# Optimization experiments

Hardware: AMD Instinct MI355X
Metric: run time of the kernel (lower is better)

## Reference

```python
import jax, jax.numpy as jnp
import numpy as np

B, S, D, H = 2, 2048, 1024, 16
DH = D // H  # 64


def setup_inputs() -> dict:
    key = jax.random.key(0)
    ks = jax.random.split(key, 8)
    query = jax.random.normal(ks[0], (B, S, D), jnp.float32)
    k_in = jax.random.normal(ks[1], (B, S, D), jnp.float32)
    v_in = jax.random.normal(ks[2], (B, S, D), jnp.float32)
    mask = jnp.zeros((B, 1, 1, S), jnp.float32)  # padding mask (0 = keep)
    # distance-based attention penalty mask: |i-j| normalized
    idx = jnp.arange(S, dtype=jnp.float32)
    att_pen_mask = jnp.abs(idx[:, None] - idx[None, :])[None, None] / S
    scale = 1.0 / np.sqrt(D)
    Wq = jax.random.normal(ks[3], (D, D), jnp.float32) * scale
    Wk = jax.random.normal(ks[4], (D, D), jnp.float32) * scale
    Wv = jax.random.normal(ks[5], (D, D), jnp.float32) * scale
    Wo = jax.random.normal(ks[6], (D, D), jnp.float32) * scale
    bo = jnp.zeros((D,), jnp.float32)
    return {"query": query, "key": k_in, "value": v_in, "mask": mask,
            "att_pen_mask": att_pen_mask, "attention_dropout": 0,
            "Wq": Wq, "Wk": Wk, "Wv": Wv, "Wo": Wo, "bo": bo}


def _split_heads(x):
    # [B,S,D] -> [B,H,S,DH]
    return x.reshape(B, S, H, DH).transpose(0, 2, 1, 3)


def reference(query, key, value, mask, att_pen_mask, attention_dropout, Wq, Wk, Wv, Wo, bo):
    q = _split_heads(query @ Wq)
    k = _split_heads(key @ Wk)
    v = _split_heads(value @ Wv)
    # scaled dot-product attention with penalty + padding mask
    scores = jnp.einsum('bhqd,bhkd->bhqk', q, k) / jnp.sqrt(jnp.float32(DH))
    scores = scores - jnp.log1p(att_pen_mask)          # distance penalty
    scores = scores + mask * (-1e9)                    # padding mask
    attn = jax.nn.softmax(scores, axis=-1)
    # attention_dropout==0 -> no dropout (matches 0 < rate < 1 gate)
    ctx = jnp.einsum('bhqk,bhkd->bhqd', attn, v)       # [B,H,S,DH]
    ctx = ctx.transpose(0, 2, 1, 3).reshape(B, S, D)
    out = ctx @ Wo + bo
    return out, attn
```

## Files before the change

### kernel.cpp

```cpp
#include <hip/hip_runtime.h>
#include <math.h>

#define BB 2
#define SS 2048
#define DD 1024
#define HH 16
#define DHH 64

typedef _Float16 f16;
typedef f16 f16x8 __attribute__((ext_vector_type(8)));
typedef f16 f16x4 __attribute__((ext_vector_type(4)));
typedef float f32x4 __attribute__((ext_vector_type(4)));
typedef float fvec4 __attribute__((ext_vector_type(4)));

#define LOG2E 1.4426950408889634f

static __device__ __forceinline__ f32x4 mfma16(f16x8 a, f16x8 b, f32x4 c) {
    return __builtin_amdgcn_mfma_f32_16x16x32_f16(a, b, c, 0, 0, 0);
}

#define SWZ(r, c) ((c) ^ (((r) & 7) << 3))

static __device__ __forceinline__ void gload_lds16(const void* g, void* l) {
    __builtin_amdgcn_global_load_lds(
        (const __attribute__((address_space(1))) void*)g,
        (__attribute__((address_space(3))) void*)l, 16, 0, 0);
}

static __device__ __forceinline__ void barrier_raw() {
    __builtin_amdgcn_sched_barrier(0);
    __builtin_amdgcn_s_barrier();
    __builtin_amdgcn_sched_barrier(0);
}
static __device__ __forceinline__ void barrier_lds() {
    asm volatile("s_waitcnt lgkmcnt(0)" ::: "memory");
    __builtin_amdgcn_s_barrier();
    __builtin_amdgcn_sched_barrier(0);
}

__global__ __launch_bounds__(256) void wtrans_kernel(
    const float* __restrict__ w0, const float* __restrict__ w1,
    const float* __restrict__ w2, const float* __restrict__ w3,
    f16* __restrict__ o0, f16* __restrict__ o1,
    f16* __restrict__ o2, f16* __restrict__ o3)
{
    const float* src; f16* dst;
    switch (blockIdx.z) {
        case 0:  src = w0; dst = o0; break;
        case 1:  src = w1; dst = o1; break;
        case 2:  src = w2; dst = o2; break;
        default: src = w3; dst = o3; break;
    }
    __shared__ float t[64][65];
    const int tid = threadIdx.x;
    const int n0 = blockIdx.x * 64, k0 = blockIdx.y * 64;
    const int r = tid >> 4, c4 = (tid & 15) * 4;
    #pragma unroll
    for (int p = 0; p < 4; ++p) {
        int row = r + p * 16;
        fvec4 v = *(const fvec4*)&src[(size_t)(k0 + row) * DD + n0 + c4];
        #pragma unroll
        for (int j = 0; j < 4; ++j) t[row][c4 + j] = v[j];
    }
    __syncthreads();
    #pragma unroll
    for (int p = 0; p < 4; ++p) {
        int row = r + p * 16;
        f16x4 v;
        #pragma unroll
        for (int j = 0; j < 4; ++j) v[j] = (f16)t[c4 + j][row];
        *(f16x4*)&dst[(size_t)(n0 + row) * DD + k0 + c4] = v;
    }
}

__global__ __launch_bounds__(256) void gemm_qkv(
    const float* __restrict__ Aq, const float* __restrict__ Ak, const float* __restrict__ Av,
    const f16* __restrict__ Wqt, const f16* __restrict__ Wkt, const f16* __restrict__ Wvt,
    f16* __restrict__ oq, f16* __restrict__ ok, f16* __restrict__ ovt)
{
    const int K = DD;
    const int l = (blockIdx.x & 7) * 96 + (blockIdx.x >> 3);
    const int z  = (l % 96) / 32;
    const int mt = (l / 96) * 4 + (l % 32) / 8;
    const int nt = l % 8;

    const float* A; const f16* Bt; f16* C;
    switch (z) {
        case 0:  A = Aq; Bt = Wqt; C = oq; break;
        case 1:  A = Ak; Bt = Wkt; C = ok; break;
        default: A = Av; Bt = Wvt; C = ovt; break;
    }
    const int m0 = mt * 128, n0 = nt * 128;
    const int tid = threadIdx.x, lane = tid & 63;
    const int wm = (tid >> 7) & 1, wn = (tid >> 6) & 1;
    const int ln = lane & 15, lg = lane >> 4;

    __shared__ f16 As[128 * 64];
    __shared__ f16 Bs[128 * 64];

    f32x4 acc[4][4] = {};

    const int sr = tid >> 3;
    const int sc = (tid & 7) * 8;
    const int l8 = sr & 7;
    const int bsrc = ((tid & 7) ^ l8) * 8;
    const int ldsbase = (sr & ~7) * 64;

    for (int k0 = 0; k0 < K; k0 += 64) {
        #pragma unroll
        for (int p = 0; p < 4; ++p)
            gload_lds16(Bt + (size_t)(n0 + sr + p * 32) * K + k0 + bsrc,
                        &Bs[ldsbase + p * 32 * 64]);
        #pragma unroll
        for (int p = 0; p < 4; ++p) {
            int row = sr + p * 32;
            const float* s = A + (size_t)(m0 + row) * K + k0 + sc;
            fvec4 x0 = *(const fvec4*)s;
            fvec4 x1 = *(const fvec4*)(s + 4);
            f16x8 v;
            #pragma unroll
            for (int j = 0; j < 4; ++j) { v[j] = (f16)x0[j]; v[j + 4] = (f16)x1[j]; }
            *(f16x8*)&As[row * 64 + SWZ(row, sc)] = v;
        }
        __syncthreads();
        #pragma unroll
        for (int ks = 0; ks < 2; ++ks) {
            f16x8 af[4], bf[4];
            #pragma unroll
            for (int i = 0; i < 4; ++i) {
                int ra = wm * 64 + i * 16 + ln, rb = wn * 64 + i * 16 + ln;
                int cc = ks * 32 + lg * 8;
                af[i] = *(const f16x8*)&As[ra * 64 + SWZ(ra, cc)];
                bf[i] = *(const f16x8*)&Bs[rb * 64 + SWZ(rb, cc)];
            }
            __builtin_amdgcn_s_setprio(1);
            #pragma unroll
            for (int i = 0; i < 4; ++i)
                #pragma unroll
                for (int j = 0; j < 4; ++j)
                    acc[i][j] = mfma16(af[i], bf[j], acc[i][j]);
            __builtin_amdgcn_s_setprio(0);
        }
        __syncthreads();
    }

    const int vmode = (z == 2);
    #pragma unroll
    for (int i = 0; i < 4; ++i) {
        #pragma unroll
        for (int j = 0; j < 4; ++j) {
            if (vmode) {
                int m = m0 + wm * 64 + i * 16 + lg * 4;
                int n = n0 + wn * 64 + j * 16 + ln;
                int b = m >> 11, s = m & (SS - 1);
                int h = n >> 6, dh = n & 63;
                f16x4 v4;
                #pragma unroll
                for (int v = 0; v < 4; ++v) v4[v] = (f16)acc[i][j][v];
                *(f16x4*)&C[((size_t)((b * HH + h) * DHH + dh)) * SS + s] = v4;
            } else {
                #pragma unroll
                for (int v = 0; v < 4; ++v) {
                    int m = m0 + wm * 64 + i * 16 + lg * 4 + v;
                    int n = n0 + wn * 64 + j * 16 + ln;
                    int b = m >> 11, s = m & (SS - 1);
                    int h = n >> 6, dh = n & 63;
                    C[((size_t)((b * HH + h) * SS + s)) * DHH + dh] = (f16)acc[i][j][v];
                }
            }
        }
    }
}

__global__ __launch_bounds__(256) void gemm_out(
    const f16* __restrict__ A, const f16* __restrict__ Bt,
    const float* __restrict__ bias, float* __restrict__ C)
{
    const int K = DD;
    const int l = (blockIdx.x & 7) * 32 + (blockIdx.x >> 3);
    const int mt = (l / 32) * 4 + (l % 32) / 8;
    const int nt = l % 8;
    const int m0 = mt * 128, n0 = nt * 128;
    const int tid = threadIdx.x, lane = tid & 63;
    const int wm = (tid >> 7) & 1, wn = (tid >> 6) & 1;
    const int ln = lane & 15, lg = lane >> 4;

    __shared__ f16 As[128 * 64];
    __shared__ f16 Bs[128 * 64];

    f32x4 acc[4][4] = {};

    const int sr = tid >> 3;
    const int l8 = sr & 7;
    const int bsrc = ((tid & 7) ^ l8) * 8;
    const int ldsbase = (sr & ~7) * 64;

    for (int k0 = 0; k0 < K; k0 += 64) {
        #pragma unroll
        for (int p = 0; p < 4; ++p) {
            gload_lds16(A + (size_t)(m0 + sr + p * 32) * K + k0 + bsrc,
                        &As[ldsbase + p * 32 * 64]);
            gload_lds16(Bt + (size_t)(n0 + sr + p * 32) * K + k0 + bsrc,
                        &Bs[ldsbase + p * 32 * 64]);
        }
        __syncthreads();
        #pragma unroll
        for (int ks = 0; ks < 2; ++ks) {
            f16x8 af[4], bf[4];
            #pragma unroll
            for (int i = 0; i < 4; ++i) {
                int ra = wm * 64 + i * 16 + ln, rb = wn * 64 + i * 16 + ln;
                int cc = ks * 32 + lg * 8;
                af[i] = *(const f16x8*)&As[ra * 64 + SWZ(ra, cc)];
                bf[i] = *(const f16x8*)&Bs[rb * 64 + SWZ(rb, cc)];
            }
            __builtin_amdgcn_s_setprio(1);
            #pragma unroll
            for (int i = 0; i < 4; ++i)
                #pragma unroll
                for (int j = 0; j < 4; ++j)
                    acc[i][j] = mfma16(af[i], bf[j], acc[i][j]);
            __builtin_amdgcn_s_setprio(0);
        }
        __syncthreads();
    }

    #pragma unroll
    for (int i = 0; i < 4; ++i)
        #pragma unroll
        for (int j = 0; j < 4; ++j)
            #pragma unroll
            for (int v = 0; v < 4; ++v) {
                int m = m0 + wm * 64 + i * 16 + lg * 4 + v;
                int n = n0 + wn * 64 + j * 16 + ln;
                C[(size_t)m * DD + n] = acc[i][j][v] + bias[n];
            }
}

__global__ __launch_bounds__(256, 4) void attn_kernel(
    const f16* __restrict__ qg, const f16* __restrict__ kg, const f16* __restrict__ vtg,
    const float* __restrict__ maskg, const float* __restrict__ peng,
    float* __restrict__ attn_out, f16* __restrict__ ctx_out)
{
    const int bid = blockIdx.x;
    const int wg = (bid & 7) * 128 + (bid >> 3);
    const int bh = wg >> 5;
    const int b = bh >> 4, h = bh & 15;
    const int q0 = (wg & 31) * 64;

    const int tid = threadIdx.x, lane = tid & 63, wv = tid >> 6;
    const int ln = lane & 15, lg = lane >> 4;

    __shared__ f16 Kt[64 * 64];
    __shared__ f16 Vt[64 * 64];
    __shared__ f16 Ps[64 * 64];
    __shared__ f16 mrowh[SS];

    for (int i = tid; i < SS; i += 256)
        mrowh[i] = (f16)fmaxf(maskg[b * SS + i] * (-1e9f * LOG2E), -60000.f);

    const f16* qbase = qg + ((size_t)bh * SS + q0 + wv * 16 + ln) * DHH;
    f16x8 aq0 = *(const f16x8*)(qbase + lg * 8);
    f16x8 aq1 = *(const f16x8*)(qbase + 32 + lg * 8);

    const f16* kbase = kg + (size_t)bh * SS * DHH;
    const f16* vbase = vtg + (size_t)bh * DHH * SS;

    const int krow = tid >> 3, kcol = (tid & 7) * 8;
    f16x8 kst0, kst1, vst0, vst1;

    #define LOADK(kt) { kst0 = *(const f16x8*)(kbase + ((size_t)(kt) * 64 + krow) * DHH + kcol); \
                        kst1 = *(const f16x8*)(kbase + ((size_t)(kt) * 64 + krow + 32) * DHH + kcol); }
    #define WRITEK()  { *(f16x8*)&Kt[krow * 64 + SWZ(krow, kcol)] = kst0; \
                        *(f16x8*)&Kt[(krow + 32) * 64 + SWZ(krow + 32, kcol)] = kst1; }
    #define LOADV(kt) { vst0 = *(const f16x8*)(vbase + (size_t)krow * SS + (kt) * 64 + kcol); \
                        vst1 = *(const f16x8*)(vbase + (size_t)(krow + 32) * SS + (kt) * 64 + kcol); }
    #define WRITEV()  { *(f16x8*)&Vt[krow * 64 + SWZ(krow, kcol)] = vst0; \
                        *(f16x8*)&Vt[(krow + 32) * 64 + SWZ(krow + 32, kcol)] = vst1; }

    const int q = q0 + wv * 16 + ln;
    const float SC = 0.125f * LOG2E;

    LOADK(0);
    WRITEK();
    __syncthreads();

    float lrun = 0.f;

    for (int kt = 0; kt < 32; ++kt) {
        if (kt < 31) LOADK(kt + 1);

        float sum = 0.f;
        #pragma unroll
        for (int sub = 0; sub < 4; ++sub) {
            int kr = sub * 16 + ln;
            f16x8 k0 = *(const f16x8*)&Kt[kr * 64 + SWZ(kr, lg * 8)];
            f16x8 k1 = *(const f16x8*)&Kt[kr * 64 + SWZ(kr, 32 + lg * 8)];
            f32x4 sa = {0.f, 0.f, 0.f, 0.f};
            __builtin_amdgcn_s_setprio(1);
            sa = mfma16(k0, aq0, sa);
            sa = mfma16(k1, aq1, sa);
            __builtin_amdgcn_s_setprio(0);
            const int kjb = kt * 64 + sub * 16 + lg * 4;
            f16x4 mr = *(const f16x4*)&mrowh[kjb];
            #pragma unroll
            for (int v = 0; v < 4; ++v) {
                int d = q - (kjb + v); d = d < 0 ? -d : d;
                sum += __builtin_amdgcn_exp2f(
                    sa[v] * SC + (float)mr[v] - __builtin_amdgcn_logf((float)(SS + d)));
            }
        }
        sum += __shfl_xor(sum, 16);
        sum += __shfl_xor(sum, 32);
        lrun += sum;

        barrier_raw();
        if (kt < 31) WRITEK();
        barrier_lds();
    }

    const float cfix = __builtin_amdgcn_logf(lrun);

    f32x4 cacc[4] = {};

    LOADK(0); LOADV(0);
    WRITEK(); WRITEV();
    __syncthreads();

    for (int kt = 0; kt < 32; ++kt) {
        if (kt < 31) { LOADK(kt + 1); LOADV(kt + 1); }

        #pragma unroll
        for (int sub = 0; sub < 4; ++sub) {
            int kr = sub * 16 + ln;
            f16x8 k0 = *(const f16x8*)&Kt[kr * 64 + SWZ(kr, lg * 8)];
            f16x8 k1 = *(const f16x8*)&Kt[kr * 64 + SWZ(kr, 32 + lg * 8)];
            f32x4 sa = {0.f, 0.f, 0.f, 0.f};
            __builtin_amdgcn_s_setprio(1);
            sa = mfma16(k0, aq0, sa);
            sa = mfma16(k1, aq1, sa);
            __builtin_amdgcn_s_setprio(0);
            const int kjb = kt * 64 + sub * 16 + lg * 4;
            f16x4 mr = *(const f16x4*)&mrowh[kjb];
            f32x4 p;
            #pragma unroll
            for (int v = 0; v < 4; ++v) {
                int d = q - (kjb + v); d = d < 0 ? -d : d;
                p[v] = __builtin_amdgcn_exp2f(
                    sa[v] * SC + (float)mr[v]
                    - __builtin_amdgcn_logf((float)(SS + d)) - cfix);
            }
            __builtin_nontemporal_store(
                p, (fvec4*)(attn_out + ((size_t)bh * SS + q) * SS + kjb));
            f16x4 pc;
            #pragma unroll
            for (int v = 0; v < 4; ++v) pc[v] = (f16)p[v];
            const int prow = wv * 16 + ln;
            *(f16x4*)&Ps[prow * 64 + SWZ(prow, sub * 16 + lg * 4)] = pc;
        }
        #pragma unroll
        for (int ks = 0; ks < 2; ++ks) {
            const int prow = wv * 16 + ln;
            f16x8 ap = *(const f16x8*)&Ps[prow * 64 + SWZ(prow, ks * 32 + lg * 8)];
            f16x8 bv0 = *(const f16x8*)&Vt[(0 * 16 + ln) * 64 + SWZ(0 * 16 + ln, ks * 32 + lg * 8)];
            f16x8 bv1 = *(const f16x8*)&Vt[(1 * 16 + ln) * 64 + SWZ(1 * 16 + ln, ks * 32 + lg * 8)];
            f16x8 bv2 = *(const f16x8*)&Vt[(2 * 16 + ln) * 64 + SWZ(2 * 16 + ln, ks * 32 + lg * 8)];
            f16x8 bv3 = *(const f16x8*)&Vt[(3 * 16 + ln) * 64 + SWZ(3 * 16 + ln, ks * 32 + lg * 8)];
            __builtin_amdgcn_s_setprio(1);
            cacc[0] = mfma16(ap, bv0, cacc[0]);
            cacc[1] = mfma16(ap, bv1, cacc[1]);
            cacc[2] = mfma16(ap, bv2, cacc[2]);
            cacc[3] = mfma16(ap, bv3, cacc[3]);
            __builtin_amdgcn_s_setprio(0);
        }

        barrier_raw();
        if (kt < 31) { WRITEK(); WRITEV(); }
        barrier_lds();
    }

    #pragma unroll
    for (int nsub = 0; nsub < 4; ++nsub) {
        #pragma unroll
        for (int v = 0; v < 4; ++v) {
            int s = q0 + wv * 16 + lg * 4 + v;
            ctx_out[(size_t)(b * SS + s) * DD + h * DHH + nsub * 16 + ln] = (f16)cacc[nsub][v];
        }
    }
    #undef LOADK
    #undef WRITEK
    #undef LOADV
    #undef WRITEV
}

extern "C" void kernel_launch(void* const* d_in, const int* in_sizes, int n_in,
                              void* d_out, int out_size, void* d_ws, size_t ws_size,
                              hipStream_t stream)
{
    const float* query = (const float*)d_in[0];
    const float* key   = (const float*)d_in[1];
    const float* value = (const float*)d_in[2];
    const float* mask  = (const float*)d_in[3];
    const float* pen   = (const float*)d_in[4];
    const float* Wq = (const float*)d_in[6];
    const float* Wk = (const float*)d_in[7];
    const float* Wv = (const float*)d_in[8];
    const float* Wo = (const float*)d_in[9];
    const float* bo = (const float*)d_in[10];

    char* ws = (char*)d_ws;
    f16* Wqt   = (f16*)(ws);
    f16* Wkt   = (f16*)(ws + (2ull << 20));
    f16* Wvt   = (f16*)(ws + (4ull << 20));
    f16* Wot   = (f16*)(ws + (6ull << 20));
    f16* qbuf  = (f16*)(ws + (8ull << 20));
    f16* kbuf  = (f16*)(ws + (16ull << 20));
    f16* vtbuf = (f16*)(ws + (24ull << 20));
    f16* ctx   = (f16*)(ws + (32ull << 20));

    float* out_main = (float*)d_out;
    float* attn_out = (float*)d_out + (size_t)BB * SS * DD;

    wtrans_kernel<<<dim3(16, 16, 4), 256, 0, stream>>>(Wq, Wk, Wv, Wo, Wqt, Wkt, Wvt, Wot);
    gemm_qkv<<<dim3(768), 256, 0, stream>>>(query, key, value, Wqt, Wkt, Wvt, qbuf, kbuf, vtbuf);
    attn_kernel<<<dim3(1024), 256, 0, stream>>>(qbuf, kbuf, vtbuf, mask, pen, attn_out, ctx);
    gemm_out<<<dim3(256), 256, 0, stream>>>(ctx, Wot, bo, out_main);
}
```

Before: 282.2 us.

## Split attention waves 2x2 over queries and keys, use reciprocal penalty factor

```diff
diff --git a/kernel.cpp b/kernel.cpp
--- a/kernel.cpp
+++ b/kernel.cpp
@@ -248,20 +248,26 @@
     const int b = bh >> 4, h = bh & 15;
     const int q0 = (wg & 31) * 64;
 
-    const int tid = threadIdx.x, lane = tid & 63, wv = tid >> 6;
+    const int tid = threadIdx.x, lane = tid & 63;
+    const int wq = tid >> 7, wk = (tid >> 6) & 1;
     const int ln = lane & 15, lg = lane >> 4;
 
-    __shared__ f16 Kt[64 * 64];
-    __shared__ f16 Vt[64 * 64];
-    __shared__ f16 Ps[64 * 64];
+    __shared__ f16 arena[12288];
     __shared__ f16 mrowh[SS];
+    f16* const Kt = arena;
+    f16* const Vt = arena + 4096;
+    f16* const Ps = arena + 8192;
 
     for (int i = tid; i < SS; i += 256)
         mrowh[i] = (f16)fmaxf(maskg[b * SS + i] * (-1e9f * LOG2E), -60000.f);
 
-    const f16* qbase = qg + ((size_t)bh * SS + q0 + wv * 16 + ln) * DHH;
-    f16x8 aq0 = *(const f16x8*)(qbase + lg * 8);
-    f16x8 aq1 = *(const f16x8*)(qbase + 32 + lg * 8);
+    f16x8 aq0[2], aq1[2];
+    #pragma unroll
+    for (int g = 0; g < 2; ++g) {
+        const f16* qb = qg + ((size_t)bh * SS + q0 + wq * 32 + g * 16 + ln) * DHH;
+        aq0[g] = *(const f16x8*)(qb + lg * 8);
+        aq1[g] = *(const f16x8*)(qb + 32 + lg * 8);
+    }
 
     const f16* kbase = kg + (size_t)bh * SS * DHH;
     const f16* vbase = vtg + (size_t)bh * DHH * SS;
@@ -278,50 +284,67 @@
     #define WRITEV()  { *(f16x8*)&Vt[krow * 64 + SWZ(krow, kcol)] = vst0; \
                         *(f16x8*)&Vt[(krow + 32) * 64 + SWZ(krow + 32, kcol)] = vst1; }
 
-    const int q = q0 + wv * 16 + ln;
     const float SC = 0.125f * LOG2E;
 
     LOADK(0);
     WRITEK();
     __syncthreads();
 
-    float lrun = 0.f;
+    float lsum[2] = {0.f, 0.f};
 
     for (int kt = 0; kt < 32; ++kt) {
         if (kt < 31) LOADK(kt + 1);
 
-        float sum = 0.f;
-        #pragma unroll
-        for (int sub = 0; sub < 4; ++sub) {
-            int kr = sub * 16 + ln;
+        #pragma unroll
+        for (int ksub = 0; ksub < 2; ++ksub) {
+            const int sub = wk * 2 + ksub;
+            const int kr = sub * 16 + ln;
             f16x8 k0 = *(const f16x8*)&Kt[kr * 64 + SWZ(kr, lg * 8)];
             f16x8 k1 = *(const f16x8*)&Kt[kr * 64 + SWZ(kr, 32 + lg * 8)];
-            f32x4 sa = {0.f, 0.f, 0.f, 0.f};
-            __builtin_amdgcn_s_setprio(1);
-            sa = mfma16(k0, aq0, sa);
-            sa = mfma16(k1, aq1, sa);
-            __builtin_amdgcn_s_setprio(0);
             const int kjb = kt * 64 + sub * 16 + lg * 4;
             f16x4 mr = *(const f16x4*)&mrowh[kjb];
             #pragma unroll
-            for (int v = 0; v < 4; ++v) {
-                int d = q - (kjb + v); d = d < 0 ? -d : d;
-                sum += __builtin_amdgcn_exp2f(
-                    sa[v] * SC + (float)mr[v] - __builtin_amdgcn_logf((float)(SS + d)));
-            }
-        }
-        sum += __shfl_xor(sum, 16);
-        sum += __shfl_xor(sum, 32);
-        lrun += sum;
-
+            for (int g = 0; g < 2; ++g) {
+                f32x4 sa = {0.f, 0.f, 0.f, 0.f};
+                __builtin_amdgcn_s_setprio(1);
+                sa = mfma16(k0, aq0[g], sa);
+                sa = mfma16(k1, aq1[g], sa);
+                __builtin_amdgcn_s_setprio(0);
+                const int qq = q0 + wq * 32 + g * 16 + ln;
+                #pragma unroll
+                for (int v = 0; v < 4; ++v) {
+                    int d = qq - (kjb + v); d = d < 0 ? -d : d;
+                    lsum[g] += __builtin_amdgcn_exp2f(sa[v] * SC + (float)mr[v])
+                             * __builtin_amdgcn_rcpf((float)(SS + d));
+                }
+            }
+        }
         barrier_raw();
         if (kt < 31) WRITEK();
         barrier_lds();
     }
 
-    const float cfix = __builtin_amdgcn_logf(lrun);
-
-    f32x4 cacc[4] = {};
+    float cfix[2];
+    {
+        #pragma unroll
+        for (int g = 0; g < 2; ++g) {
+            lsum[g] += __shfl_xor(lsum[g], 16);
+            lsum[g] += __shfl_xor(lsum[g], 32);
+        }
+        float* lred = (float*)Ps;
+        if (lg == 0) {
+            lred[wk * 64 + wq * 32 + ln]      = lsum[0];
+            lred[wk * 64 + wq * 32 + 16 + ln] = lsum[1];
+        }
+        __syncthreads();
+        #pragma unroll
+        for (int g = 0; g < 2; ++g)
+            cfix[g] = __builtin_amdgcn_logf(
+                lred[wq * 32 + g * 16 + ln] + lred[64 + wq * 32 + g * 16 + ln]);
+        __syncthreads();
+    }
+
+    f32x4 cacc[2][4] = {};
 
     LOADK(0); LOADV(0);
     WRITEK(); WRITEV();
@@ -331,61 +354,86 @@
         if (kt < 31) { LOADK(kt + 1); LOADV(kt + 1); }
 
         #pragma unroll
-        for (int sub = 0; sub < 4; ++sub) {
-            int kr = sub * 16 + ln;
+        for (int ksub = 0; ksub < 2; ++ksub) {
+            const int sub = wk * 2 + ksub;
+            const int kr = sub * 16 + ln;
             f16x8 k0 = *(const f16x8*)&Kt[kr * 64 + SWZ(kr, lg * 8)];
             f16x8 k1 = *(const f16x8*)&Kt[kr * 64 + SWZ(kr, 32 + lg * 8)];
-            f32x4 sa = {0.f, 0.f, 0.f, 0.f};
-            __builtin_amdgcn_s_setprio(1);
-            sa = mfma16(k0, aq0, sa);
-            sa = mfma16(k1, aq1, sa);
-            __builtin_amdgcn_s_setprio(0);
             const int kjb = kt * 64 + sub * 16 + lg * 4;
             f16x4 mr = *(const f16x4*)&mrowh[kjb];
-            f32x4 p;
-            #pragma unroll
-            for (int v = 0; v < 4; ++v) {
-                int d = q - (kjb + v); d = d < 0 ? -d : d;
-                p[v] = __builtin_amdgcn_exp2f(
-                    sa[v] * SC + (float)mr[v]
-                    - __builtin_amdgcn_logf((float)(SS + d)) - cfix);
-            }
-            __builtin_nontemporal_store(
-                p, (fvec4*)(attn_out + ((size_t)bh * SS + q) * SS + kjb));
-            f16x4 pc;
-            #pragma unroll
-            for (int v = 0; v < 4; ++v) pc[v] = (f16)p[v];
-            const int prow = wv * 16 + ln;
-            *(f16x4*)&Ps[prow * 64 + SWZ(prow, sub * 16 + lg * 4)] = pc;
-        }
-        #pragma unroll
-        for (int ks = 0; ks < 2; ++ks) {
-            const int prow = wv * 16 + ln;
-            f16x8 ap = *(const f16x8*)&Ps[prow * 64 + SWZ(prow, ks * 32 + lg * 8)];
-            f16x8 bv0 = *(const f16x8*)&Vt[(0 * 16 + ln) * 64 + SWZ(0 * 16 + ln, ks * 32 + lg * 8)];
-            f16x8 bv1 = *(const f16x8*)&Vt[(1 * 16 + ln) * 64 + SWZ(1 * 16 + ln, ks * 32 + lg * 8)];
-            f16x8 bv2 = *(const f16x8*)&Vt[(2 * 16 + ln) * 64 + SWZ(2 * 16 + ln, ks * 32 + lg * 8)];
-            f16x8 bv3 = *(const f16x8*)&Vt[(3 * 16 + ln) * 64 + SWZ(3 * 16 + ln, ks * 32 + lg * 8)];
-            __builtin_amdgcn_s_setprio(1);
-            cacc[0] = mfma16(ap, bv0, cacc[0]);
-            cacc[1] = mfma16(ap, bv1, cacc[1]);
-            cacc[2] = mfma16(ap, bv2, cacc[2]);
-            cacc[3] = mfma16(ap, bv3, cacc[3]);
-            __builtin_amdgcn_s_setprio(0);
+            #pragma unroll
+            for (int g = 0; g < 2; ++g) {
+                f32x4 sa = {0.f, 0.f, 0.f, 0.f};
+                __builtin_amdgcn_s_setprio(1);
+                sa = mfma16(k0, aq0[g], sa);
+                sa = mfma16(k1, aq1[g], sa);
+                __builtin_amdgcn_s_setprio(0);
+                const int qq = q0 + wq * 32 + g * 16 + ln;
+                f32x4 p;
+                #pragma unroll
+                for (int v = 0; v < 4; ++v) {
+                    int d = qq - (kjb + v); d = d < 0 ? -d : d;
+                    p[v] = __builtin_amdgcn_exp2f(sa[v] * SC + (float)mr[v] - cfix[g])
+                         * __builtin_amdgcn_rcpf((float)(SS + d));
+                }
+                __builtin_nontemporal_store(
+                    p, (fvec4*)(attn_out + ((size_t)bh * SS + qq) * SS + kjb));
+                f16x4 pc;
+                #pragma unroll
+                for (int v = 0; v < 4; ++v) pc[v] = (f16)p[v];
+                const int prow = wq * 32 + g * 16 + ln;
+                *(f16x4*)&Ps[prow * 64 + SWZ(prow, sub * 16 + lg * 4)] = pc;
+            }
+        }
+        {
+            f16x8 bv[4];
+            #pragma unroll
+            for (int nsub = 0; nsub < 4; ++nsub) {
+                int vr = nsub * 16 + ln;
+                bv[nsub] = *(const f16x8*)&Vt[vr * 64 + SWZ(vr, wk * 32 + lg * 8)];
+            }
+            #pragma unroll
+            for (int g = 0; g < 2; ++g) {
+                const int prow = wq * 32 + g * 16 + ln;
+                f16x8 ap = *(const f16x8*)&Ps[prow * 64 + SWZ(prow, wk * 32 + lg * 8)];
+                __builtin_amdgcn_s_setprio(1);
+                #pragma unroll
+                for (int nsub = 0; nsub < 4; ++nsub)
+                    cacc[g][nsub] = mfma16(ap, bv[nsub], cacc[g][nsub]);
+                __builtin_amdgcn_s_setprio(0);
+            }
         }
 
         barrier_raw();
-        if (kt < 31) { WRITEK(); WRITEV(); }
+        if (kt < 31) { LOADK(kt + 1); WRITEK(); WRITEV(); }
         barrier_lds();
     }
 
-    #pragma unroll
-    for (int nsub = 0; nsub < 4; ++nsub) {
-        #pragma unroll
-        for (int v = 0; v < 4; ++v) {
-            int s = q0 + wv * 16 + lg * 4 + v;
-            ctx_out[(size_t)(b * SS + s) * DD + h * DHH + nsub * 16 + ln] = (f16)cacc[nsub][v];
-        }
+    __syncthreads();
+    float* red = (float*)arena;
+    if (wk == 1) {
+        #pragma unroll
+        for (int g = 0; g < 2; ++g)
+            #pragma unroll
+            for (int nsub = 0; nsub < 4; ++nsub)
+                #pragma unroll
+                for (int v = 0; v < 4; ++v)
+                    red[(wq * 32 + g * 16 + lg * 4 + v) * 64 + nsub * 16 + ln] =
+                        cacc[g][nsub][v];
+    }
+    __syncthreads();
+    if (wk == 0) {
+        #pragma unroll
+        for (int g = 0; g < 2; ++g)
+            #pragma unroll
+            for (int nsub = 0; nsub < 4; ++nsub)
+                #pragma unroll
+                for (int v = 0; v < 4; ++v) {
+                    float s = cacc[g][nsub][v]
+                            + red[(wq * 32 + g * 16 + lg * 4 + v) * 64 + nsub * 16 + ln];
+                    int sq = q0 + wq * 32 + g * 16 + lg * 4 + v;
+                    ctx_out[(size_t)(b * SS + sq) * DD + h * DHH + nsub * 16 + ln] = (f16)s;
+                }
     }
     #undef LOADK
     #undef WRITEK
```

Result: faster. 275.1 us (-2.5%).
